# Performance work log

Hardware: AMD Instinct MI355X
Metric: run time of the kernel (lower is better)

## Reference

```python
import jax, jax.numpy as jnp
import numpy as np

K = 10

def _lrelu(v):
    return jax.nn.leaky_relu(v, negative_slope=0.2)

def _knn_idx(x, k):
    # x: [B, C, N]; returns indices of k nearest neighbors [B, N, k]
    xx = jnp.sum(x * x, axis=1, keepdims=True)          # [B,1,N]
    inner = -2.0 * jnp.einsum('bcn,bcm->bnm', x, x)     # [B,N,N]
    pd = -xx - inner - jnp.swapaxes(xx, 1, 2)           # -squared distance [B,N,N]
    _, idx = jax.lax.top_k(pd, k)
    return idx

def _graph_feature(x, k):
    # x: [B, C, N] -> edge features [B, 2C, N, k]
    idx = _knn_idx(x, k)                                # [B,N,k]
    xt = jnp.swapaxes(x, 1, 2)                          # [B,N,C]
    feat = jax.vmap(lambda xb, ib: xb[ib])(xt, idx)     # [B,N,k,C] gather
    center = xt[:, :, None, :]                          # [B,N,1,C]
    f = jnp.concatenate([feat - center,
                         jnp.broadcast_to(center, feat.shape)], axis=-1)  # [B,N,k,2C]
    return jnp.transpose(f, (0, 3, 1, 2))               # [B,2C,N,k]

def _edge_block(x, W, k):
    # conv2d 1x1 (no bias) + LeakyReLU + max over neighbors
    g = _graph_feature(x, k)                            # [B,2C,N,k]
    h = _lrelu(jnp.einsum('oc,bcnk->bonk', W, g))
    return jnp.max(h, axis=-1)                          # [B,O,N]

def setup_inputs() -> dict:
    key = jax.random.key(0)
    ks = jax.random.split(key, 9)
    def w(k_, *shape):
        fan_in = shape[-1]
        return jax.random.normal(k_, shape, dtype=jnp.float32) / np.sqrt(fan_in)
    return {
        'x':  jax.random.normal(ks[0], (8, 3, 2048), dtype=jnp.float32),
        'W1': w(ks[1], 64, 6),
        'W2': w(ks[2], 64, 128),
        'W3': w(ks[3], 128, 128),
        'W4': w(ks[4], 256, 256),
        'W5': w(ks[5], 512, 512),
        'L1': w(ks[6], 512, 1024),
        'L2': w(ks[7], 256, 512),
        'b2': jnp.zeros((256,), dtype=jnp.float32),
    }

def reference(x, W1, W2, W3, W4, W5, L1, L2, b2):
    x1 = _edge_block(x,  W1, K)   # [B,64,N]
    x2 = _edge_block(x1, W2, K)   # [B,64,N]
    x3 = _edge_block(x2, W3, K)   # [B,128,N]
    x4 = _edge_block(x3, W4, K)   # [B,256,N]
    h = jnp.concatenate([x1, x2, x3, x4], axis=1)        # [B,512,N]
    h = _lrelu(jnp.einsum('oc,bcn->bon', W5, h))         # [B,512,N]
    hmax = jnp.max(h, axis=-1)                           # [B,512]
    havg = jnp.mean(h, axis=-1)                          # [B,512]
    f = jnp.concatenate([hmax, havg], axis=1)            # [B,1024]
    f = _lrelu(f @ L1.T)                                 # [B,512]
    out = _lrelu(f @ L2.T + b2)                          # [B,256]
    return out
```

## Files before the change

### kernel.cpp

```cpp
#include <hip/hip_runtime.h>
#include <cstdint>
#include <cstddef>

constexpr int B_ = 8;
constexpr int N_ = 2048;
constexpr int K_ = 10;

typedef __attribute__((ext_vector_type(8))) short bf16x8;
typedef __attribute__((ext_vector_type(4))) float f32x4;

__device__ __forceinline__ float lrelu(float v) { return fmaxf(v, 0.2f * v); }

__device__ __forceinline__ short f2bf(float f) {
    uint32_t u = __builtin_bit_cast(uint32_t, f);
    u += 0x7fff + ((u >> 16) & 1);
    return (short)(u >> 16);
}
__device__ __forceinline__ float bf2f(short s) {
    uint32_t x = ((uint32_t)(unsigned short)s) << 16;
    return __builtin_bit_cast(float, x);
}

__global__ void k_transpose(const float* __restrict__ x, float* __restrict__ xt) {
    int i = blockIdx.x * 256 + threadIdx.x;
    if (i >= B_ * N_) return;
    int b = i / N_, n = i % N_;
#pragma unroll
    for (int c = 0; c < 3; ++c)
        xt[(size_t)i * 3 + c] = x[((size_t)b * 3 + c) * N_ + n];
}

__global__ void k_cvt(const float* __restrict__ W4, const float* __restrict__ W5,
                      short* __restrict__ Wb4, short* __restrict__ W5b) {
    int i = blockIdx.x * 256 + threadIdx.x;
    if (i < 256 * 128) {
        Wb4[i] = f2bf(W4[(size_t)(i >> 7) * 256 + (i & 127)]);
    } else {
        int k = i - 256 * 128;
        if (k < 512 * 512) W5b[k] = f2bf(W5[k]);
    }
}

__global__ void k_norms(const float* __restrict__ xt, int LD, int OFF, int C,
                        float* __restrict__ nrm) {
    int gid = blockIdx.x * 256 + threadIdx.x;
    int wid = gid >> 6;
    int lane = threadIdx.x & 63;
    if (wid >= B_ * N_) return;
    const float* row = xt + (size_t)wid * LD + OFF;
    float s = 0.f;
    for (int c = lane; c < C; c += 64) { float v = row[c]; s += v * v; }
#pragma unroll
    for (int off = 32; off; off >>= 1) s += __shfl_down(s, off);
    if (lane == 0) nrm[wid] = s;
}

__global__ __launch_bounds__(256) void k_knn3(const float* __restrict__ x,
                                              int* __restrict__ idxout) {
    __shared__ float xs[3][N_];
    __shared__ float ns[N_];
    const int b = blockIdx.x;
    const int w = threadIdx.x >> 6, lane = threadIdx.x & 63;
    const int n = blockIdx.y * 4 + w;
    for (int e = threadIdx.x; e < 3 * N_; e += 256)
        xs[e / N_][e % N_] = x[(size_t)b * 3 * N_ + e];
    __syncthreads();
    for (int m = threadIdx.x; m < N_; m += 256) {
        float a0 = xs[0][m], a1 = xs[1][m], a2 = xs[2][m];
        ns[m] = a0 * a0 + a1 * a1 + a2 * a2;
    }
    __syncthreads();
    const float q0 = xs[0][n], q1 = xs[1][n], q2 = xs[2][n];

    float sv[32];
#pragma unroll
    for (int g = 0; g < 32; ++g) {
        int m = g * 64 + lane;
        sv[g] = 2.f * (q0 * xs[0][m] + q1 * xs[1][m] + q2 * xs[2][m]) - ns[m];
    }
    float lm = sv[0];
#pragma unroll
    for (int g = 1; g < 32; ++g) lm = fmaxf(lm, sv[g]);
    float cur = lm, T = lm;
#pragma unroll
    for (int i = 0; i < K_; ++i) {
        float wm = cur;
#pragma unroll
        for (int off = 1; off < 64; off <<= 1) wm = fmaxf(wm, __shfl_xor(wm, off));
        T = wm;
        unsigned long long m = __ballot(cur == wm);
        int first = __ffsll(m) - 1;
        if (lane == first) cur = -INFINITY;
    }
    float kv[K_]; int ki[K_];
#pragma unroll
    for (int i = 0; i < K_; ++i) { kv[i] = -INFINITY; ki[i] = 0x7fffffff; }
#pragma unroll
    for (int g = 0; g < 32; ++g) {
        unsigned long long mk = __ballot(sv[g] >= T && sv[g] > kv[0]);
        while (mk) {
            int l = __ffsll(mk) - 1;
            mk &= mk - 1;
            float v = __shfl(sv[g], l);
            if (v > kv[0]) {
                kv[0] = v; ki[0] = g * 64 + l;
#pragma unroll
                for (int u = 0; u < K_ - 1; ++u)
                    if (kv[u] > kv[u + 1]) {
                        float tv = kv[u]; kv[u] = kv[u + 1]; kv[u + 1] = tv;
                        int tix = ki[u]; ki[u] = ki[u + 1]; ki[u + 1] = tix;
                    }
            }
        }
    }
    if (lane == 0) {
        int* op = idxout + ((size_t)b * N_ + n) * K_;
#pragma unroll
        for (int k = 0; k < K_; ++k) op[k] = ki[K_ - 1 - k];
    }
}

template <int C>
__global__ __launch_bounds__(256) void k_scores_mfma(const float* __restrict__ xt, int LD, int OFF,
                                                     const float* __restrict__ nrm,
                                                     float* __restrict__ S, int b0) {
    constexpr int RPC = C / 64;
    constexpr int NCH = 3 * RPC;
    constexpr int T = N_ / 64;
    __shared__ short AN[64 * 64];
    __shared__ short AM[64 * 64];
    const int bl = blockIdx.x;
    const int b = b0 + bl;
    int p = blockIdx.y;
    int r0 = 0, off = 0;
    while (off + (T - r0) <= p) { off += T - r0; ++r0; }
    const int ti = r0, tj = r0 + (p - off);
    const int n0 = ti * 64, m0 = tj * 64;
    const int t = threadIdx.x;
    const int lane = t & 63, w = t >> 6;
    const int colg = lane & 15, kg = lane >> 4;
    const float* xb = xt + ((size_t)b * N_) * LD + OFF;
    const float* nb = nrm + (size_t)b * N_;
    float* Sb = S + (size_t)bl * N_ * N_;

    f32x4 acc[4];
#pragma unroll
    for (int j = 0; j < 4; ++j) acc[j] = (f32x4){0.f, 0.f, 0.f, 0.f};

    for (int ch = 0; ch < NCH; ++ch) {
        const int region = ch / RPC;
        const int cc0 = (ch % RPC) * 64;
        __syncthreads();
#pragma unroll
        for (int e = 0; e < 4; ++e) {
            int idx = t + e * 256;
            int r = idx >> 4, q = idx & 15;
            float4 vn = *(const float4*)&xb[(size_t)(n0 + r) * LD + cc0 + q * 4];
            float4 vm = *(const float4*)&xb[(size_t)(m0 + r) * LD + cc0 + q * 4];
            float an4[4] = {vn.x, vn.y, vn.z, vn.w};
            float am4[4] = {vm.x, vm.y, vm.z, vm.w};
            short sa[4], sb[4];
#pragma unroll
            for (int c2 = 0; c2 < 4; ++c2) {
                short hn = f2bf(an4[c2]);
                short hm = f2bf(am4[c2]);
                sa[c2] = (region == 1) ? f2bf(an4[c2] - bf2f(hn)) : hn;
                sb[c2] = (region == 2) ? f2bf(am4[c2] - bf2f(hm)) : hm;
            }
            int base16 = r * 128 + (q >> 1) * 16;
            int byte = (base16 ^ ((r & 7) << 4)) + (q & 1) * 8;
            *(short4*)((char*)AN + byte) = make_short4(sa[0], sa[1], sa[2], sa[3]);
            *(short4*)((char*)AM + byte) = make_short4(sb[0], sb[1], sb[2], sb[3]);
        }
        __syncthreads();
        const int arow = w * 16 + colg;
#pragma unroll
        for (int s = 0; s < 2; ++s) {
            int abyte = (arow * 128 + s * 64 + kg * 16) ^ ((arow & 7) << 4);
            bf16x8 af = *(const bf16x8*)((const char*)AN + abyte);
#pragma unroll
            for (int j = 0; j < 4; ++j) {
                int brow = j * 16 + colg;
                int bbyte = (brow * 128 + s * 64 + kg * 16) ^ ((brow & 7) << 4);
                bf16x8 bfr = *(const bf16x8*)((const char*)AM + bbyte);
                acc[j] = __builtin_amdgcn_mfma_f32_16x16x32_bf16(af, bfr, acc[j], 0, 0, 0);
            }
        }
    }
#pragma unroll
    for (int j = 0; j < 4; ++j) {
        float nm = nb[m0 + j * 16 + colg];
#pragma unroll
        for (int r = 0; r < 4; ++r) {
            int row = n0 + w * 16 + kg * 4 + r;
            Sb[(size_t)row * N_ + m0 + j * 16 + colg] = 2.f * acc[j][r] - nm;
        }
    }
    if (ti != tj) {
#pragma unroll
        for (int r = 0; r < 4; ++r) {
            int nrow = n0 + w * 16 + kg * 4 + r;
            float nn = nb[nrow];
#pragma unroll
            for (int j = 0; j < 4; ++j)
                Sb[(size_t)(m0 + j * 16 + colg) * N_ + nrow] = 2.f * acc[j][r] - nn;
        }
    }
}

__global__ __launch_bounds__(256) void k_topk(const float* __restrict__ S,
                                              int* __restrict__ idxout, int b0) {
    const int bl = blockIdx.x, b = b0 + bl;
    const int wv = threadIdx.x >> 6, lane = threadIdx.x & 63;
    const int n = blockIdx.y * 4 + wv;
    const float* row = S + (size_t)bl * N_ * N_ + (size_t)n * N_;

    float sv[32];
#pragma unroll
    for (int g = 0; g < 32; ++g) sv[g] = __builtin_nontemporal_load(&row[g * 64 + lane]);

    float lm = sv[0];
#pragma unroll
    for (int g = 1; g < 32; ++g) lm = fmaxf(lm, sv[g]);

    float cur = lm, T = lm;
#pragma unroll
    for (int i = 0; i < K_; ++i) {
        float wm = cur;
#pragma unroll
        for (int off = 1; off < 64; off <<= 1) wm = fmaxf(wm, __shfl_xor(wm, off));
        T = wm;
        unsigned long long m = __ballot(cur == wm);
        int first = __ffsll(m) - 1;
        if (lane == first) cur = -INFINITY;
    }

    float kv[K_]; int ki[K_];
#pragma unroll
    for (int i = 0; i < K_; ++i) { kv[i] = -INFINITY; ki[i] = 0x7fffffff; }

#pragma unroll
    for (int g = 0; g < 32; ++g) {
        unsigned long long mk = __ballot(sv[g] >= T && sv[g] > kv[0]);
        while (mk) {
            int l = __ffsll(mk) - 1;
            mk &= mk - 1;
            float v = __shfl(sv[g], l);
            if (v > kv[0]) {
                kv[0] = v; ki[0] = g * 64 + l;
#pragma unroll
                for (int u = 0; u < K_ - 1; ++u)
                    if (kv[u] > kv[u + 1]) {
                        float tv = kv[u]; kv[u] = kv[u + 1]; kv[u + 1] = tv;
                        int tix = ki[u]; ki[u] = ki[u + 1]; ki[u + 1] = tix;
                    }
            }
        }
    }
    if (lane == 0) {
        int* op = idxout + ((size_t)b * N_ + n) * K_;
#pragma unroll
        for (int k = 0; k < K_; ++k) op[k] = ki[K_ - 1 - k];
    }
}

template <int C, int O>
__global__ __launch_bounds__(256) void k_center(const float* __restrict__ xt, int LD, int OFF,
                                                const float* __restrict__ W,
                                                float* __restrict__ tbuf) {
    constexpr int KC = (C == 3) ? 4 : 32;
    __shared__ __align__(16) float XT[64][36];
    __shared__ __align__(16) float WDT[KC][68];
    const int b = blockIdx.x;
    const int n0 = blockIdx.y * 64;
    const int ob = blockIdx.z * 64;
    const int t = threadIdx.x;
    const int tn = t & 15, to = t >> 4;
    const float* xb = xt + ((size_t)b * N_) * LD + OFF;
    float4 acc[4];
#pragma unroll
    for (int i = 0; i < 4; ++i) acc[i] = make_float4(0, 0, 0, 0);
    for (int c0 = 0; c0 < C; c0 += KC) {
        __syncthreads();
        for (int e = t; e < 64 * KC; e += 256) {
            int r = e / KC, cc = e % KC;
            XT[r][cc] = (C == 3) ? ((cc < 3) ? xb[(size_t)(n0 + r) * LD + cc] : 0.f)
                                 : xb[(size_t)(n0 + r) * LD + c0 + cc];
        }
        for (int e = t; e < 64 * KC; e += 256) {
            int oo = e / KC, cc = e % KC;
            float wd, wc;
            if (C == 3) {
                wd = (cc < 3) ? W[(ob + oo) * 6 + cc] : 0.f;
                wc = (cc < 3) ? W[(ob + oo) * 6 + 3 + cc] : 0.f;
            } else {
                wd = W[(size_t)(ob + oo) * (2 * C) + c0 + cc];
                wc = W[(size_t)(ob + oo) * (2 * C) + C + c0 + cc];
            }
            WDT[cc][oo] = wc - wd;
        }
        __syncthreads();
#pragma unroll 4
        for (int cc = 0; cc < KC; ++cc) {
            float4 w4 = *(const float4*)&WDT[cc][to * 4];
#pragma unroll
            for (int i = 0; i < 4; ++i) {
                float a = XT[tn * 4 + i][cc];
                acc[i].x += a * w4.x; acc[i].y += a * w4.y;
                acc[i].z += a * w4.z; acc[i].w += a * w4.w;
            }
        }
    }
#pragma unroll
    for (int i = 0; i < 4; ++i)
        *(float4*)&tbuf[((size_t)b * N_ + n0 + tn * 4 + i) * O + ob + to * 4] = acc[i];
}

template <int C, int O>
__global__ __launch_bounds__(256) void k_conv(const float* __restrict__ xt, int LDI, int OFFI,
                                              const int* __restrict__ idx,
                                              const float* __restrict__ W,
                                              const float* __restrict__ tbuf,
                                              float* __restrict__ hout, int OFFO) {
    constexpr int KC = (C == 3) ? 4 : 32;
    __shared__ __align__(16) float A[160][36];
    __shared__ __align__(16) float WT[KC][68];
    __shared__ int nb_s[160];
    const int b = blockIdx.x;
    const int n0 = blockIdx.y * 16;
    const int t = threadIdx.x;
    const int p = t >> 4, og = t & 15;
    if (t < 160) nb_s[t] = idx[((size_t)b * N_ + n0 + t / K_) * K_ + (t % K_)];
    const float* xb = xt + ((size_t)b * N_) * LDI + OFFI;

    for (int ob = 0; ob < O; ob += 64) {
        float4 acc[K_];
#pragma unroll
        for (int j = 0; j < K_; ++j) acc[j] = make_float4(0, 0, 0, 0);
        for (int c0 = 0; c0 < C; c0 += KC) {
            __syncthreads();
            if (C == 3) {
                for (int e = t; e < 160 * 4; e += 256) {
                    int r = e / 4, cc = e % 4;
                    A[r][cc] = (cc < 3) ? xb[(size_t)nb_s[r] * LDI + cc] : 0.f;
                }
            } else {
                for (int e = t; e < 160 * 8; e += 256) {
                    int r = e / 8, c4 = e % 8;
                    *(float4*)&A[r][c4 * 4] =
                        *(const float4*)&xb[(size_t)nb_s[r] * LDI + c0 + c4 * 4];
                }
            }
            for (int e = t; e < 64 * KC; e += 256) {
                int oo = e / KC, cc = e % KC;
                float w;
                if (C == 3) w = (cc < 3) ? W[(ob + oo) * 6 + cc] : 0.f;
                else        w = W[(size_t)(ob + oo) * (2 * C) + c0 + cc];
                WT[cc][oo] = w;
            }
            __syncthreads();
#pragma unroll 4
            for (int cc = 0; cc < KC; ++cc) {
                float4 w4 = *(const float4*)&WT[cc][og * 4];
#pragma unroll
                for (int j = 0; j < K_; ++j) {
                    float a = A[p * K_ + j][cc];
                    acc[j].x += a * w4.x; acc[j].y += a * w4.y;
                    acc[j].z += a * w4.z; acc[j].w += a * w4.w;
                }
            }
        }
        float4 tv = *(const float4*)&tbuf[((size_t)b * N_ + n0 + p) * O + ob + og * 4];
        float4 mx = acc[0];
#pragma unroll
        for (int j = 1; j < K_; ++j) {
            mx.x = fmaxf(mx.x, acc[j].x); mx.y = fmaxf(mx.y, acc[j].y);
            mx.z = fmaxf(mx.z, acc[j].z); mx.w = fmaxf(mx.w, acc[j].w);
        }
        float4 r;
        r.x = lrelu(mx.x + tv.x); r.y = lrelu(mx.y + tv.y);
        r.z = lrelu(mx.z + tv.z); r.w = lrelu(mx.w + tv.w);
        *(float4*)&hout[((size_t)b * N_ + n0 + p) * 512 + OFFO + ob + og * 4] = r;
    }
}

__global__ __launch_bounds__(256) void k_conv4_mfma(const float* __restrict__ hcat,
                                                    const int* __restrict__ idx,
                                                    const short* __restrict__ Wb,
                                                    const float* __restrict__ tbuf,
                                                    float* __restrict__ hout) {
    __shared__ short Ab[160 * 128];
    __shared__ int nb_s[160];
    const int b = blockIdx.x;
    const int n0 = blockIdx.y * 16;
    const int t = threadIdx.x;
    const int lane = t & 63, wv = t >> 6;
    const int colg = lane & 15, kg = lane >> 4;
    if (t < 160) nb_s[t] = idx[((size_t)b * N_ + n0 + t / K_) * K_ + (t % K_)];
    __syncthreads();
    for (int e = t; e < 160 * 32; e += 256) {
        int r = e >> 5, q = e & 31;
        const float4 v = *(const float4*)&hcat[((size_t)b * N_ + nb_s[r]) * 512 + 128 + q * 4];
        short4 s4 = { f2bf(v.x), f2bf(v.y), f2bf(v.z), f2bf(v.w) };
        int byte = r * 256 + ((q * 8) ^ (((r / K_) & 7) << 4));
        *(short4*)((char*)Ab + byte) = s4;
    }
    bf16x8 bf[4][4];
    const int ob = wv * 64;
#pragma unroll
    for (int nt = 0; nt < 4; ++nt)
#pragma unroll
        for (int ks = 0; ks < 4; ++ks)
            bf[nt][ks] = *(const bf16x8*)&Wb[(size_t)(ob + nt * 16 + colg) * 128 + ks * 32 + kg * 8];
    __syncthreads();

    f32x4 macc[4];
#pragma unroll
    for (int nt = 0; nt < 4; ++nt)
        macc[nt] = (f32x4){-INFINITY, -INFINITY, -INFINITY, -INFINITY};

    const int arow = colg * K_;
    const int aswz = (colg & 7) << 4;
#pragma unroll
    for (int j = 0; j < K_; ++j) {
        f32x4 acc[4];
#pragma unroll
        for (int nt = 0; nt < 4; ++nt) acc[nt] = (f32x4){0.f, 0.f, 0.f, 0.f};
#pragma unroll
        for (int ks = 0; ks < 4; ++ks) {
            int byte = (arow + j) * 256 + (((ks * 32 + kg * 8) * 2) ^ aswz);
            bf16x8 af = *(const bf16x8*)((const char*)Ab + byte);
#pragma unroll
            for (int nt = 0; nt < 4; ++nt)
                acc[nt] = __builtin_amdgcn_mfma_f32_16x16x32_bf16(af, bf[nt][ks], acc[nt], 0, 0, 0);
        }
#pragma unroll
        for (int nt = 0; nt < 4; ++nt) {
            macc[nt].x = fmaxf(macc[nt].x, acc[nt].x);
            macc[nt].y = fmaxf(macc[nt].y, acc[nt].y);
            macc[nt].z = fmaxf(macc[nt].z, acc[nt].z);
            macc[nt].w = fmaxf(macc[nt].w, acc[nt].w);
        }
    }
#pragma unroll
    for (int nt = 0; nt < 4; ++nt)
#pragma unroll
        for (int r = 0; r < 4; ++r) {
            int p = kg * 4 + r;
            int o = ob + nt * 16 + colg;
            float v = macc[nt][r] + tbuf[((size_t)b * N_ + n0 + p) * 256 + o];
            hout[((size_t)b * N_ + n0 + p) * 512 + 256 + o] = lrelu(v);
        }
}

__global__ __launch_bounds__(256) void k_final_mfma(const float* __restrict__ hcat,
                                                    const short* __restrict__ W5b,
                                                    float* __restrict__ pmax,
                                                    float* __restrict__ psum) {
    __shared__ short Ab[64 * 128];
    const int b = blockIdx.x, nc = blockIdx.y, obk = blockIdx.z;
    const int n0 = nc * 64, ob = obk * 64;
    const int t = threadIdx.x, lane = t & 63, wv = t >> 6;
    const int colg = lane & 15, kg = lane >> 4;
    const int o = ob + wv * 16 + colg;

    f32x4 acc[4];
#pragma unroll
    for (int mt = 0; mt < 4; ++mt) acc[mt] = (f32x4){0.f, 0.f, 0.f, 0.f};

    for (int kc = 0; kc < 4; ++kc) {
        __syncthreads();
        for (int e = t; e < 64 * 32; e += 256) {
            int r = e >> 5, q = e & 31;
            const float4 v = *(const float4*)&hcat[((size_t)b * N_ + n0 + r) * 512 + kc * 128 + q * 4];
            short4 s4 = { f2bf(v.x), f2bf(v.y), f2bf(v.z), f2bf(v.w) };
            int byte = r * 256 + ((q * 8) ^ ((r & 7) << 4));
            *(short4*)((char*)Ab + byte) = s4;
        }
        __syncthreads();
#pragma unroll
        for (int ks = 0; ks < 4; ++ks) {
            bf16x8 bfrag = *(const bf16x8*)&W5b[(size_t)o * 512 + kc * 128 + ks * 32 + kg * 8];
#pragma unroll
            for (int mt = 0; mt < 4; ++mt) {
                int row = mt * 16 + colg;
                int byte = row * 256 + (((ks * 32 + kg * 8) * 2) ^ ((row & 7) << 4));
                bf16x8 af = *(const bf16x8*)((const char*)Ab + byte);
                acc[mt] = __builtin_amdgcn_mfma_f32_16x16x32_bf16(af, bfrag, acc[mt], 0, 0, 0);
            }
        }
    }
    float mx = -INFINITY, sm = 0.f;
#pragma unroll
    for (int mt = 0; mt < 4; ++mt)
#pragma unroll
        for (int r = 0; r < 4; ++r) {
            float v = lrelu(acc[mt][r]);
            mx = fmaxf(mx, v); sm += v;
        }
    mx = fmaxf(mx, __shfl_xor(mx, 16)); sm += __shfl_xor(sm, 16);
    mx = fmaxf(mx, __shfl_xor(mx, 32)); sm += __shfl_xor(sm, 32);
    if (lane < 16) {
        pmax[((size_t)b * 512 + ob + wv * 16 + lane) * 32 + nc] = mx;
        psum[((size_t)b * 512 + ob + wv * 16 + lane) * 32 + nc] = sm;
    }
}

__global__ __launch_bounds__(256) void k_pool(const float* __restrict__ pmax,
                                              const float* __restrict__ psum,
                                              float* __restrict__ f) {
    int i = blockIdx.x * 256 + threadIdx.x;
    if (i >= B_ * 512) return;
    int b = i >> 9, o = i & 511;
    const float* pm = pmax + (size_t)i * 32;
    const float* ps = psum + (size_t)i * 32;
    float mm = -INFINITY, ss = 0.f;
#pragma unroll
    for (int q = 0; q < 32; ++q) { mm = fmaxf(mm, pm[q]); ss += ps[q]; }
    f[(size_t)b * 1024 + o] = mm;
    f[(size_t)b * 1024 + 512 + o] = ss * (1.0f / 2048.0f);
}

__global__ __launch_bounds__(256) void k_fc1(const float* __restrict__ f,
                                             const float* __restrict__ L1,
                                             float* __restrict__ f1) {
    __shared__ float fs[8][1024];
    const int t = threadIdx.x, lane = t & 63, w = t >> 6;
    for (int e = t; e < 2048; e += 256)
        *(float4*)&fs[0][e * 4] = *(const float4*)&f[e * 4];
    __syncthreads();
    const int o = blockIdx.x * 4 + w;
    float acc[8];
#pragma unroll
    for (int b = 0; b < 8; ++b) acc[b] = 0.f;
    const float* Lrow = L1 + (size_t)o * 1024;
#pragma unroll
    for (int e = 0; e < 16; ++e) {
        float wv = Lrow[e * 64 + lane];
#pragma unroll
        for (int b = 0; b < 8; ++b) acc[b] += wv * fs[b][e * 64 + lane];
    }
#pragma unroll
    for (int off = 32; off; off >>= 1)
#pragma unroll
        for (int b = 0; b < 8; ++b) acc[b] += __shfl_xor(acc[b], off);
#pragma unroll
    for (int b = 0; b < 8; ++b)
        if (lane == b) f1[(size_t)b * 512 + o] = lrelu(acc[b]);
}

__global__ __launch_bounds__(256) void k_fc2(const float* __restrict__ f1,
                                             const float* __restrict__ L2,
                                             const float* __restrict__ b2,
                                             float* __restrict__ out) {
    __shared__ float fs[8][512];
    const int t = threadIdx.x, lane = t & 63, w = t >> 6;
    for (int e = t; e < 1024; e += 256)
        *(float4*)&fs[0][e * 4] = *(const float4*)&f1[e * 4];
    __syncthreads();
    const int o = blockIdx.x * 4 + w;
    float acc[8];
#pragma unroll
    for (int b = 0; b < 8; ++b) acc[b] = 0.f;
    const float* Lrow = L2 + (size_t)o * 512;
#pragma unroll
    for (int e = 0; e < 8; ++e) {
        float wv = Lrow[e * 64 + lane];
#pragma unroll
        for (int b = 0; b < 8; ++b) acc[b] += wv * fs[b][e * 64 + lane];
    }
#pragma unroll
    for (int off = 32; off; off >>= 1)
#pragma unroll
        for (int b = 0; b < 8; ++b) acc[b] += __shfl_xor(acc[b], off);
    float bb = b2[o];
#pragma unroll
    for (int b = 0; b < 8; ++b)
        if (lane == b) out[(size_t)b * 256 + o] = lrelu(acc[b] + bb);
}

extern "C" void kernel_launch(void* const* d_in, const int* in_sizes, int n_in,
                              void* d_out, int out_size, void* d_ws, size_t ws_size,
                              hipStream_t stream) {
    (void)in_sizes; (void)n_in; (void)out_size;
    const float* x  = (const float*)d_in[0];
    const float* W1 = (const float*)d_in[1];
    const float* W2 = (const float*)d_in[2];
    const float* W3 = (const float*)d_in[3];
    const float* W4 = (const float*)d_in[4];
    const float* W5 = (const float*)d_in[5];
    const float* L1 = (const float*)d_in[6];
    const float* L2 = (const float*)d_in[7];
    const float* b2 = (const float*)d_in[8];
    float* out = (float*)d_out;

    float* ws   = (float*)d_ws;
    float* xt   = ws;
    float* nrm  = xt + (size_t)B_ * N_ * 3;
    int*   idxb = (int*)(nrm + (size_t)B_ * N_);
    float* tb   = (float*)(idxb + (size_t)B_ * N_ * K_);
    float* hcat = tb + (size_t)B_ * N_ * 256;
    float* pmax = hcat + (size_t)B_ * N_ * 512;
    float* psum = pmax + (size_t)B_ * 512 * 32;
    short* wb4  = (short*)(psum + (size_t)B_ * 512 * 32);
    short* w5b  = wb4 + 256 * 128;
    float* fbuf = (float*)(w5b + 512 * 512);
    float* f1b  = fbuf + 8192;
    float* scor = f1b + 4096;

    const size_t base_f = 49152 + 16384 + 163840 + 4194304 + 8388608 +
                          131072 + 131072 + 16384 + 131072 + 8192 + 4096;
    const size_t nsq = (size_t)N_ * N_;
    size_t avail = (ws_size / 4 > base_f) ? (ws_size / 4 - base_f) : 0;
    int CH = 1;
    if (avail >= 8 * nsq) CH = 8;
    else if (avail >= 4 * nsq) CH = 4;
    else if (avail >= 2 * nsq) CH = 2;

    constexpr int TP = (N_ / 64) * (N_ / 64 + 1) / 2;

    dim3 blk(256);
    k_transpose<<<dim3((B_ * N_ + 255) / 256), blk, 0, stream>>>(x, xt);
    k_cvt<<<dim3((256 * 128 + 512 * 512 + 255) / 256), blk, 0, stream>>>(W4, W5, wb4, w5b);

    k_knn3<<<dim3(B_, N_ / 4), blk, 0, stream>>>(x, idxb);
    k_center<3, 64><<<dim3(B_, N_ / 64, 1), blk, 0, stream>>>(xt, 3, 0, W1, tb);
    k_conv<3, 64><<<dim3(B_, N_ / 16), blk, 0, stream>>>(xt, 3, 0, idxb, W1, tb, hcat, 0);

    k_norms<<<dim3(B_ * N_ / 4), blk, 0, stream>>>(hcat, 512, 0, 64, nrm);
    for (int b0 = 0; b0 < B_; b0 += CH) {
        k_scores_mfma<64><<<dim3(CH, TP), blk, 0, stream>>>(hcat, 512, 0, nrm, scor, b0);
        k_topk<<<dim3(CH, N_ / 4), blk, 0, stream>>>(scor, idxb, b0);
    }
    k_center<64, 64><<<dim3(B_, N_ / 64, 1), blk, 0, stream>>>(hcat, 512, 0, W2, tb);
    k_conv<64, 64><<<dim3(B_, N_ / 16), blk, 0, stream>>>(hcat, 512, 0, idxb, W2, tb, hcat, 64);

    k_norms<<<dim3(B_ * N_ / 4), blk, 0, stream>>>(hcat, 512, 64, 64, nrm);
    for (int b0 = 0; b0 < B_; b0 += CH) {
        k_scores_mfma<64><<<dim3(CH, TP), blk, 0, stream>>>(hcat, 512, 64, nrm, scor, b0);
        k_topk<<<dim3(CH, N_ / 4), blk, 0, stream>>>(scor, idxb, b0);
    }
    k_center<64, 128><<<dim3(B_, N_ / 64, 2), blk, 0, stream>>>(hcat, 512, 64, W3, tb);
    k_conv<64, 128><<<dim3(B_, N_ / 16), blk, 0, stream>>>(hcat, 512, 64, idxb, W3, tb, hcat, 128);

    k_norms<<<dim3(B_ * N_ / 4), blk, 0, stream>>>(hcat, 512, 128, 128, nrm);
    for (int b0 = 0; b0 < B_; b0 += CH) {
        k_scores_mfma<128><<<dim3(CH, TP), blk, 0, stream>>>(hcat, 512, 128, nrm, scor, b0);
        k_topk<<<dim3(CH, N_ / 4), blk, 0, stream>>>(scor, idxb, b0);
    }
    k_center<128, 256><<<dim3(B_, N_ / 64, 4), blk, 0, stream>>>(hcat, 512, 128, W4, tb);
    k_conv4_mfma<<<dim3(B_, N_ / 16), blk, 0, stream>>>(hcat, idxb, wb4, tb, hcat);

    k_final_mfma<<<dim3(B_, 32, 8), blk, 0, stream>>>(hcat, w5b, pmax, psum);
    k_pool<<<dim3(B_ * 512 / 256), blk, 0, stream>>>(pmax, psum, fbuf);
    k_fc1<<<dim3(128), blk, 0, stream>>>(fbuf, L1, f1b);
    k_fc2<<<dim3(64), blk, 0, stream>>>(f1b, L2, b2, out);
}
```

Before: 544.9 us.

## Fuse kNN score GEMM with streaming top-k, split columns and merge

Replaces the separate score kernel, which wrote the full N×N distance matrix, and the top-k kernel that read it back, with one kernel. Each block computes 64-row score tiles with MFMA and keeps a running per-row top-10 in shared memory. Columns are split across CS=2 blocks and a small merge kernel combines the partial lists. This removes the large score-matrix traffic and the batching loop, but it drops the symmetric tile reuse, so the dot-product work doubles, and it adds a serial per-row insertion loop within each wave.

```diff
diff --git a/kernel.cpp b/kernel.cpp
--- a/kernel.cpp
+++ b/kernel.cpp
@@ -120,147 +120,139 @@
     }
 }
 
-template <int C>
-__global__ __launch_bounds__(256) void k_scores_mfma(const float* __restrict__ xt, int LD, int OFF,
-                                                     const float* __restrict__ nrm,
-                                                     float* __restrict__ S, int b0) {
+template <int C, int CS>
+__global__ __launch_bounds__(256) void k_knn_fmfma(const float* __restrict__ xt, int LD, int OFF,
+                                                   const float* __restrict__ nrm,
+                                                   float* __restrict__ pv, int* __restrict__ pi) {
     constexpr int RPC = C / 64;
     constexpr int NCH = 3 * RPC;
-    constexpr int T = N_ / 64;
+    constexpr int COLS = N_ / CS;
+    constexpr int NT = COLS / 64;
     __shared__ short AN[64 * 64];
     __shared__ short AM[64 * 64];
-    const int bl = blockIdx.x;
-    const int b = b0 + bl;
-    int p = blockIdx.y;
-    int r0 = 0, off = 0;
-    while (off + (T - r0) <= p) { off += T - r0; ++r0; }
-    const int ti = r0, tj = r0 + (p - off);
-    const int n0 = ti * 64, m0 = tj * 64;
+    __shared__ float SCN[4][16][65];
+    __shared__ float KV[64][10];
+    __shared__ int   KI[64][10];
+    const int b = blockIdx.x;
+    const int n0 = blockIdx.y * 64;
+    const int cs = blockIdx.z;
     const int t = threadIdx.x;
     const int lane = t & 63, w = t >> 6;
     const int colg = lane & 15, kg = lane >> 4;
     const float* xb = xt + ((size_t)b * N_) * LD + OFF;
     const float* nb = nrm + (size_t)b * N_;
-    float* Sb = S + (size_t)bl * N_ * N_;
-
-    f32x4 acc[4];
-#pragma unroll
-    for (int j = 0; j < 4; ++j) acc[j] = (f32x4){0.f, 0.f, 0.f, 0.f};
-
-    for (int ch = 0; ch < NCH; ++ch) {
-        const int region = ch / RPC;
-        const int cc0 = (ch % RPC) * 64;
-        __syncthreads();
-#pragma unroll
-        for (int e = 0; e < 4; ++e) {
-            int idx = t + e * 256;
-            int r = idx >> 4, q = idx & 15;
-            float4 vn = *(const float4*)&xb[(size_t)(n0 + r) * LD + cc0 + q * 4];
-            float4 vm = *(const float4*)&xb[(size_t)(m0 + r) * LD + cc0 + q * 4];
-            float an4[4] = {vn.x, vn.y, vn.z, vn.w};
-            float am4[4] = {vm.x, vm.y, vm.z, vm.w};
-            short sa[4], sb[4];
-#pragma unroll
-            for (int c2 = 0; c2 < 4; ++c2) {
-                short hn = f2bf(an4[c2]);
-                short hm = f2bf(am4[c2]);
-                sa[c2] = (region == 1) ? f2bf(an4[c2] - bf2f(hn)) : hn;
-                sb[c2] = (region == 2) ? f2bf(am4[c2] - bf2f(hm)) : hm;
-            }
-            int base16 = r * 128 + (q >> 1) * 16;
-            int byte = (base16 ^ ((r & 7) << 4)) + (q & 1) * 8;
-            *(short4*)((char*)AN + byte) = make_short4(sa[0], sa[1], sa[2], sa[3]);
-            *(short4*)((char*)AM + byte) = make_short4(sb[0], sb[1], sb[2], sb[3]);
-        }
-        __syncthreads();
-        const int arow = w * 16 + colg;
-#pragma unroll
-        for (int s = 0; s < 2; ++s) {
-            int abyte = (arow * 128 + s * 64 + kg * 16) ^ ((arow & 7) << 4);
-            bf16x8 af = *(const bf16x8*)((const char*)AN + abyte);
-#pragma unroll
-            for (int j = 0; j < 4; ++j) {
-                int brow = j * 16 + colg;
-                int bbyte = (brow * 128 + s * 64 + kg * 16) ^ ((brow & 7) << 4);
-                bf16x8 bfr = *(const bf16x8*)((const char*)AM + bbyte);
-                acc[j] = __builtin_amdgcn_mfma_f32_16x16x32_bf16(af, bfr, acc[j], 0, 0, 0);
-            }
-        }
-    }
-#pragma unroll
-    for (int j = 0; j < 4; ++j) {
-        float nm = nb[m0 + j * 16 + colg];
-#pragma unroll
-        for (int r = 0; r < 4; ++r) {
-            int row = n0 + w * 16 + kg * 4 + r;
-            Sb[(size_t)row * N_ + m0 + j * 16 + colg] = 2.f * acc[j][r] - nm;
-        }
-    }
-    if (ti != tj) {
-#pragma unroll
-        for (int r = 0; r < 4; ++r) {
-            int nrow = n0 + w * 16 + kg * 4 + r;
-            float nn = nb[nrow];
-#pragma unroll
-            for (int j = 0; j < 4; ++j)
-                Sb[(size_t)(m0 + j * 16 + colg) * N_ + nrow] = 2.f * acc[j][r] - nn;
-        }
-    }
-}
-
-__global__ __launch_bounds__(256) void k_topk(const float* __restrict__ S,
-                                              int* __restrict__ idxout, int b0) {
-    const int bl = blockIdx.x, b = b0 + bl;
-    const int wv = threadIdx.x >> 6, lane = threadIdx.x & 63;
-    const int n = blockIdx.y * 4 + wv;
-    const float* row = S + (size_t)bl * N_ * N_ + (size_t)n * N_;
-
-    float sv[32];
-#pragma unroll
-    for (int g = 0; g < 32; ++g) sv[g] = __builtin_nontemporal_load(&row[g * 64 + lane]);
-
-    float lm = sv[0];
-#pragma unroll
-    for (int g = 1; g < 32; ++g) lm = fmaxf(lm, sv[g]);
-
-    float cur = lm, T = lm;
-#pragma unroll
-    for (int i = 0; i < K_; ++i) {
-        float wm = cur;
-#pragma unroll
-        for (int off = 1; off < 64; off <<= 1) wm = fmaxf(wm, __shfl_xor(wm, off));
-        T = wm;
-        unsigned long long m = __ballot(cur == wm);
-        int first = __ffsll(m) - 1;
-        if (lane == first) cur = -INFINITY;
-    }
-
-    float kv[K_]; int ki[K_];
-#pragma unroll
-    for (int i = 0; i < K_; ++i) { kv[i] = -INFINITY; ki[i] = 0x7fffffff; }
-
-#pragma unroll
-    for (int g = 0; g < 32; ++g) {
-        unsigned long long mk = __ballot(sv[g] >= T && sv[g] > kv[0]);
-        while (mk) {
-            int l = __ffsll(mk) - 1;
-            mk &= mk - 1;
-            float v = __shfl(sv[g], l);
-            if (v > kv[0]) {
-                kv[0] = v; ki[0] = g * 64 + l;
-#pragma unroll
-                for (int u = 0; u < K_ - 1; ++u)
-                    if (kv[u] > kv[u + 1]) {
-                        float tv = kv[u]; kv[u] = kv[u + 1]; kv[u + 1] = tv;
-                        int tix = ki[u]; ki[u] = ki[u + 1]; ki[u + 1] = tix;
+
+    for (int e = t; e < 640; e += 256) { KV[e / 10][e % 10] = -INFINITY; KI[e / 10][e % 10] = 0x7fffffff; }
+
+    for (int tile = 0; tile < NT; ++tile) {
+        const int mt0 = cs * COLS + tile * 64;
+        f32x4 acc[4];
+#pragma unroll
+        for (int j = 0; j < 4; ++j) acc[j] = (f32x4){0.f, 0.f, 0.f, 0.f};
+
+        for (int ch = 0; ch < NCH; ++ch) {
+            const int region = ch / RPC;
+            const int cc0 = (ch % RPC) * 64;
+            __syncthreads();
+#pragma unroll
+            for (int e = 0; e < 4; ++e) {
+                int idx = t + e * 256;
+                int r = idx >> 4, q = idx & 15;
+                float4 vn = *(const float4*)&xb[(size_t)(n0 + r) * LD + cc0 + q * 4];
+                float4 vm = *(const float4*)&xb[(size_t)(mt0 + r) * LD + cc0 + q * 4];
+                float an4[4] = {vn.x, vn.y, vn.z, vn.w};
+                float am4[4] = {vm.x, vm.y, vm.z, vm.w};
+                short sa[4], sb[4];
+#pragma unroll
+                for (int c2 = 0; c2 < 4; ++c2) {
+                    short hn = f2bf(an4[c2]);
+                    short hm = f2bf(am4[c2]);
+                    sa[c2] = (region == 1) ? f2bf(an4[c2] - bf2f(hn)) : hn;
+                    sb[c2] = (region == 2) ? f2bf(am4[c2] - bf2f(hm)) : hm;
+                }
+                int base16 = r * 128 + (q >> 1) * 16;
+                int byte = (base16 ^ ((r & 7) << 4)) + (q & 1) * 8;
+                *(short4*)((char*)AN + byte) = make_short4(sa[0], sa[1], sa[2], sa[3]);
+                *(short4*)((char*)AM + byte) = make_short4(sb[0], sb[1], sb[2], sb[3]);
+            }
+            __syncthreads();
+            const int arow = w * 16 + colg;
+#pragma unroll
+            for (int s = 0; s < 2; ++s) {
+                int abyte = (arow * 128 + s * 64 + kg * 16) ^ ((arow & 7) << 4);
+                bf16x8 af = *(const bf16x8*)((const char*)AN + abyte);
+#pragma unroll
+                for (int j = 0; j < 4; ++j) {
+                    int brow = j * 16 + colg;
+                    int bbyte = (brow * 128 + s * 64 + kg * 16) ^ ((brow & 7) << 4);
+                    bf16x8 bfr = *(const bf16x8*)((const char*)AM + bbyte);
+                    acc[j] = __builtin_amdgcn_mfma_f32_16x16x32_bf16(af, bfr, acc[j], 0, 0, 0);
+                }
+            }
+        }
+#pragma unroll
+        for (int j = 0; j < 4; ++j) {
+            float nm = nb[mt0 + j * 16 + colg];
+#pragma unroll
+            for (int r = 0; r < 4; ++r)
+                SCN[w][kg * 4 + r][j * 16 + colg] = 2.f * acc[j][r] - nm;
+        }
+        for (int row = 0; row < 16; ++row) {
+            const int gr = w * 16 + row;
+            float v = SCN[w][row][lane];
+            float kv0 = KV[gr][0];
+            unsigned long long mk = __ballot(v > kv0);
+            while (mk) {
+                int l = __ffsll(mk) - 1;
+                mk &= mk - 1;
+                float vv = __shfl(v, l);
+                kv0 = KV[gr][0];
+                if (vv > kv0) {
+                    float slot = (lane < 10) ? KV[gr][lane] : 0.f;
+                    unsigned long long lessm = __ballot(lane < 10 && slot < vv);
+                    int p = (int)__popcll(lessm);
+                    if (lane < 10) {
+                        float nv; int ni;
+                        if (lane < p - 1)      { nv = KV[gr][lane + 1]; ni = KI[gr][lane + 1]; }
+                        else if (lane == p - 1){ nv = vv; ni = mt0 + l; }
+                        else                   { nv = slot; ni = KI[gr][lane]; }
+                        KV[gr][lane] = nv; KI[gr][lane] = ni;
                     }
-            }
-        }
-    }
-    if (lane == 0) {
-        int* op = idxout + ((size_t)b * N_ + n) * K_;
-#pragma unroll
-        for (int k = 0; k < K_; ++k) op[k] = ki[K_ - 1 - k];
+                }
+            }
+        }
+    }
+    __syncthreads();
+    if (t < 64) {
+        float* opv = pv + (((size_t)b * N_ + n0 + t) * CS + cs) * K_;
+        int*   opi = pi + (((size_t)b * N_ + n0 + t) * CS + cs) * K_;
+#pragma unroll
+        for (int k = 0; k < K_; ++k) { opv[k] = KV[t][9 - k]; opi[k] = KI[t][9 - k]; }
+    }
+}
+
+template <int CS>
+__global__ __launch_bounds__(256) void k_kmerge(const float* __restrict__ pv,
+                                                const int* __restrict__ pi,
+                                                int* __restrict__ idxout) {
+    int row = blockIdx.x * 256 + threadIdx.x;
+    if (row >= B_ * N_) return;
+    const float* rv = pv + (size_t)row * CS * K_;
+    const int*   ri = pi + (size_t)row * CS * K_;
+    int p[CS];
+#pragma unroll
+    for (int q = 0; q < CS; ++q) p[q] = 0;
+    int* op = idxout + (size_t)row * K_;
+    for (int k = 0; k < K_; ++k) {
+        float bv = -INFINITY; int bi = 0x7fffffff, bq = 0;
+#pragma unroll
+        for (int q = 0; q < CS; ++q) {
+            float v = rv[q * K_ + p[q]];
+            int id = ri[q * K_ + p[q]];
+            if (v > bv || (v == bv && id < bi)) { bv = v; bi = id; bq = q; }
+        }
+        op[k] = bi;
+        ++p[bq];
     }
 }
 
@@ -582,7 +574,7 @@
 extern "C" void kernel_launch(void* const* d_in, const int* in_sizes, int n_in,
                               void* d_out, int out_size, void* d_ws, size_t ws_size,
                               hipStream_t stream) {
-    (void)in_sizes; (void)n_in; (void)out_size;
+    (void)in_sizes; (void)n_in; (void)out_size; (void)ws_size;
     const float* x  = (const float*)d_in[0];
     const float* W1 = (const float*)d_in[1];
     const float* W2 = (const float*)d_in[2];
@@ -593,6 +585,8 @@
     const float* L2 = (const float*)d_in[7];
     const float* b2 = (const float*)d_in[8];
     float* out = (float*)d_out;
+
+    constexpr int CS = 2;
 
     float* ws   = (float*)d_ws;
     float* xt   = ws;
@@ -606,18 +600,8 @@
     short* w5b  = wb4 + 256 * 128;
     float* fbuf = (float*)(w5b + 512 * 512);
     float* f1b  = fbuf + 8192;
-    float* scor = f1b + 4096;
-
-    const size_t base_f = 49152 + 16384 + 163840 + 4194304 + 8388608 +
-                          131072 + 131072 + 16384 + 131072 + 8192 + 4096;
-    const size_t nsq = (size_t)N_ * N_;
-    size_t avail = (ws_size / 4 > base_f) ? (ws_size / 4 - base_f) : 0;
-    int CH = 1;
-    if (avail >= 8 * nsq) CH = 8;
-    else if (avail >= 4 * nsq) CH = 4;
-    else if (avail >= 2 * nsq) CH = 2;
-
-    constexpr int TP = (N_ / 64) * (N_ / 64 + 1) / 2;
+    float* pv   = f1b + 4096;
+    int*   pi   = (int*)(pv + (size_t)B_ * N_ * CS * K_);
 
     dim3 blk(256);
     k_transpose<<<dim3((B_ * N_ + 255) / 256), blk, 0, stream>>>(x, xt);
@@ -628,26 +612,20 @@
     k_conv<3, 64><<<dim3(B_, N_ / 16), blk, 0, stream>>>(xt, 3, 0, idxb, W1, tb, hcat, 0);
 
     k_norms<<<dim3(B_ * N_ / 4), blk, 0, stream>>>(hcat, 512, 0, 64, nrm);
-    for (int b0 = 0; b0 < B_; b0 += CH) {
-        k_scores_mfma<64><<<dim3(CH, TP), blk, 0, stream>>>(hcat, 512, 0, nrm, scor, b0);
-        k_topk<<<dim3(CH, N_ / 4), blk, 0, stream>>>(scor, idxb, b0);
-    }
+    k_knn_fmfma<64, CS><<<dim3(B_, N_ / 64, CS), blk, 0, stream>>>(hcat, 512, 0, nrm, pv, pi);
+    k_kmerge<CS><<<dim3(B_ * N_ / 256), blk, 0, stream>>>(pv, pi, idxb);
     k_center<64, 64><<<dim3(B_, N_ / 64, 1), blk, 0, stream>>>(hcat, 512, 0, W2, tb);
     k_conv<64, 64><<<dim3(B_, N_ / 16), blk, 0, stream>>>(hcat, 512, 0, idxb, W2, tb, hcat, 64);
 
     k_norms<<<dim3(B_ * N_ / 4), blk, 0, stream>>>(hcat, 512, 64, 64, nrm);
-    for (int b0 = 0; b0 < B_; b0 += CH) {
-        k_scores_mfma<64><<<dim3(CH, TP), blk, 0, stream>>>(hcat, 512, 64, nrm, scor, b0);
-        k_topk<<<dim3(CH, N_ / 4), blk, 0, stream>>>(scor, idxb, b0);
-    }
+    k_knn_fmfma<64, CS><<<dim3(B_, N_ / 64, CS), blk, 0, stream>>>(hcat, 512, 64, nrm, pv, pi);
+    k_kmerge<CS><<<dim3(B_ * N_ / 256), blk, 0, stream>>>(pv, pi, idxb);
     k_center<64, 128><<<dim3(B_, N_ / 64, 2), blk, 0, stream>>>(hcat, 512, 64, W3, tb);
     k_conv<64, 128><<<dim3(B_, N_ / 16), blk, 0, stream>>>(hcat, 512, 64, idxb, W3, tb, hcat, 128);
 
     k_norms<<<dim3(B_ * N_ / 4), blk, 0, stream>>>(hcat, 512, 128, 128, nrm);
-    for (int b0 = 0; b0 < B_; b0 += CH) {
-        k_scores_mfma<128><<<dim3(CH, TP), blk, 0, stream>>>(hcat, 512, 128, nrm, scor, b0);
-        k_topk<<<dim3(CH, N_ / 4), blk, 0, stream>>>(scor, idxb, b0);
-    }
+    k_knn_fmfma<128, CS><<<dim3(B_, N_ / 64, CS), blk, 0, stream>>>(hcat, 512, 128, nrm, pv, pi);
+    k_kmerge<CS><<<dim3(B_ * N_ / 256), blk, 0, stream>>>(pv, pi, idxb);
     k_center<128, 256><<<dim3(B_, N_ / 64, 4), blk, 0, stream>>>(hcat, 512, 128, W4, tb);
     k_conv4_mfma<<<dim3(B_, N_ / 16), blk, 0, stream>>>(hcat, idxb, wb4, tb, hcat);
 
```

Result: slower. 1.368 ms (+151.0%).

## Run edge conv layers 2 and 3 on MFMA with split-bf16 precision

Applied to the files above, without the earlier changes.

Replaces the scalar FP32 neighbor convolution for blocks 2 and 3 with an MFMA kernel. Gathered neighbor features and weights are each split into bf16 high and low parts, and three bf16 MFMA products (hi*hi, lo*hi, hi*lo) approximate FP32 accuracy. The max over neighbors and the center-term add are fused into the epilogue. This adds a small weight pre-conversion kernel and swizzled LDS staging, and uses three times the MFMA work in exchange for matrix-core throughput in place of VALU FMAs.

```diff
diff --git a/kernel.cpp b/kernel.cpp
--- a/kernel.cpp
+++ b/kernel.cpp
@@ -38,6 +38,22 @@
     } else {
         int k = i - 256 * 128;
         if (k < 512 * 512) W5b[k] = f2bf(W5[k]);
+    }
+}
+
+__global__ void k_cvt2(const float* __restrict__ W2, const float* __restrict__ W3,
+                       short* __restrict__ w2h, short* __restrict__ w2l,
+                       short* __restrict__ w3h, short* __restrict__ w3l) {
+    int i = blockIdx.x * 256 + threadIdx.x;
+    if (i < 64 * 64) {
+        float v = W2[(size_t)(i >> 6) * 128 + (i & 63)];
+        short h = f2bf(v);
+        w2h[i] = h; w2l[i] = f2bf(v - bf2f(h));
+    } else if (i < 64 * 64 + 128 * 64) {
+        int k = i - 64 * 64;
+        float v = W3[(size_t)(k >> 6) * 128 + (k & 63)];
+        short h = f2bf(v);
+        w3h[k] = h; w3l[k] = f2bf(v - bf2f(h));
     }
 }
 
@@ -384,6 +400,103 @@
     }
 }
 
+template <int O>
+__global__ __launch_bounds__(256) void k_conv23_mfma(const float* __restrict__ hcat, int OFFI,
+                                                     const int* __restrict__ idx,
+                                                     const short* __restrict__ Wh,
+                                                     const short* __restrict__ Wl,
+                                                     const float* __restrict__ tbuf,
+                                                     float* __restrict__ hout, int OFFO) {
+    constexpr int CT = O / 64;
+    __shared__ short Ah[160 * 64];
+    __shared__ short Al[160 * 64];
+    __shared__ int nb_s[160];
+    const int b = blockIdx.x;
+    const int n0 = blockIdx.y * 16;
+    const int t = threadIdx.x;
+    const int lane = t & 63, wv = t >> 6;
+    const int colg = lane & 15, kg = lane >> 4;
+    if (t < 160) nb_s[t] = idx[((size_t)b * N_ + n0 + t / K_) * K_ + (t % K_)];
+    __syncthreads();
+    for (int e = t; e < 160 * 16; e += 256) {
+        int r = e >> 4, q = e & 15;
+        const float4 v = *(const float4*)&hcat[((size_t)b * N_ + nb_s[r]) * 512 + OFFI + q * 4];
+        float a4[4] = {v.x, v.y, v.z, v.w};
+        short sh[4], sl[4];
+#pragma unroll
+        for (int c2 = 0; c2 < 4; ++c2) {
+            sh[c2] = f2bf(a4[c2]);
+            sl[c2] = f2bf(a4[c2] - bf2f(sh[c2]));
+        }
+        int byte = r * 128 + ((q * 8) ^ (((r / K_) & 7) << 4));
+        *(short4*)((char*)Ah + byte) = make_short4(sh[0], sh[1], sh[2], sh[3]);
+        *(short4*)((char*)Al + byte) = make_short4(sl[0], sl[1], sl[2], sl[3]);
+    }
+    bf16x8 bh[CT][2], blo[CT][2];
+    const int obase = wv * (O / 4);
+#pragma unroll
+    for (int ct = 0; ct < CT; ++ct)
+#pragma unroll
+        for (int ks = 0; ks < 2; ++ks) {
+            int o = obase + ct * 16 + colg;
+            bh[ct][ks]  = *(const bf16x8*)&Wh[(size_t)o * 64 + ks * 32 + kg * 8];
+            blo[ct][ks] = *(const bf16x8*)&Wl[(size_t)o * 64 + ks * 32 + kg * 8];
+        }
+    __syncthreads();
+
+    f32x4 macc[CT];
+#pragma unroll
+    for (int ct = 0; ct < CT; ++ct)
+        macc[ct] = (f32x4){-INFINITY, -INFINITY, -INFINITY, -INFINITY};
+
+    const int aswz = (colg & 7) << 4;
+#pragma unroll
+    for (int j = 0; j < K_; ++j) {
+        const int arow = colg * K_ + j;
+        bf16x8 afh[2], afl[2];
+#pragma unroll
+        for (int ks = 0; ks < 2; ++ks) {
+            int byte = arow * 128 + ((ks * 64 + kg * 16) ^ aswz);
+            afh[ks] = *(const bf16x8*)((const char*)Ah + byte);
+            afl[ks] = *(const bf16x8*)((const char*)Al + byte);
+        }
+        f32x4 acc[CT];
+#pragma unroll
+        for (int ct = 0; ct < CT; ++ct) acc[ct] = (f32x4){0.f, 0.f, 0.f, 0.f};
+#pragma unroll
+        for (int ks = 0; ks < 2; ++ks)
+#pragma unroll
+            for (int ct = 0; ct < CT; ++ct)
+                acc[ct] = __builtin_amdgcn_mfma_f32_16x16x32_bf16(afh[ks], bh[ct][ks], acc[ct], 0, 0, 0);
+#pragma unroll
+        for (int ks = 0; ks < 2; ++ks)
+#pragma unroll
+            for (int ct = 0; ct < CT; ++ct)
+                acc[ct] = __builtin_amdgcn_mfma_f32_16x16x32_bf16(afl[ks], bh[ct][ks], acc[ct], 0, 0, 0);
+#pragma unroll
+        for (int ks = 0; ks < 2; ++ks)
+#pragma unroll
+            for (int ct = 0; ct < CT; ++ct)
+                acc[ct] = __builtin_amdgcn_mfma_f32_16x16x32_bf16(afh[ks], blo[ct][ks], acc[ct], 0, 0, 0);
+#pragma unroll
+        for (int ct = 0; ct < CT; ++ct) {
+            macc[ct].x = fmaxf(macc[ct].x, acc[ct].x);
+            macc[ct].y = fmaxf(macc[ct].y, acc[ct].y);
+            macc[ct].z = fmaxf(macc[ct].z, acc[ct].z);
+            macc[ct].w = fmaxf(macc[ct].w, acc[ct].w);
+        }
+    }
+#pragma unroll
+    for (int ct = 0; ct < CT; ++ct)
+#pragma unroll
+        for (int r = 0; r < 4; ++r) {
+            int p = kg * 4 + r;
+            int o = obase + ct * 16 + colg;
+            float v = macc[ct][r] + tbuf[((size_t)b * N_ + n0 + p) * O + o];
+            hout[((size_t)b * N_ + n0 + p) * 512 + OFFO + o] = lrelu(v);
+        }
+}
+
 __global__ __launch_bounds__(256) void k_conv4_mfma(const float* __restrict__ hcat,
                                                     const int* __restrict__ idx,
                                                     const short* __restrict__ Wb,
@@ -604,12 +717,16 @@
     float* psum = pmax + (size_t)B_ * 512 * 32;
     short* wb4  = (short*)(psum + (size_t)B_ * 512 * 32);
     short* w5b  = wb4 + 256 * 128;
-    float* fbuf = (float*)(w5b + 512 * 512);
+    short* w2h  = w5b + 512 * 512;
+    short* w2l  = w2h + 64 * 64;
+    short* w3h  = w2l + 64 * 64;
+    short* w3l  = w3h + 128 * 64;
+    float* fbuf = (float*)(w3l + 128 * 64);
     float* f1b  = fbuf + 8192;
     float* scor = f1b + 4096;
 
     const size_t base_f = 49152 + 16384 + 163840 + 4194304 + 8388608 +
-                          131072 + 131072 + 16384 + 131072 + 8192 + 4096;
+                          131072 + 131072 + 16384 + 131072 + 12288 + 8192 + 4096;
     const size_t nsq = (size_t)N_ * N_;
     size_t avail = (ws_size / 4 > base_f) ? (ws_size / 4 - base_f) : 0;
     int CH = 1;
@@ -622,6 +739,7 @@
     dim3 blk(256);
     k_transpose<<<dim3((B_ * N_ + 255) / 256), blk, 0, stream>>>(x, xt);
     k_cvt<<<dim3((256 * 128 + 512 * 512 + 255) / 256), blk, 0, stream>>>(W4, W5, wb4, w5b);
+    k_cvt2<<<dim3((64 * 64 + 128 * 64 + 255) / 256), blk, 0, stream>>>(W2, W3, w2h, w2l, w3h, w3l);
 
     k_knn3<<<dim3(B_, N_ / 4), blk, 0, stream>>>(x, idxb);
     k_center<3, 64><<<dim3(B_, N_ / 64, 1), blk, 0, stream>>>(xt, 3, 0, W1, tb);
@@ -633,7 +751,7 @@
         k_topk<<<dim3(CH, N_ / 4), blk, 0, stream>>>(scor, idxb, b0);
     }
     k_center<64, 64><<<dim3(B_, N_ / 64, 1), blk, 0, stream>>>(hcat, 512, 0, W2, tb);
-    k_conv<64, 64><<<dim3(B_, N_ / 16), blk, 0, stream>>>(hcat, 512, 0, idxb, W2, tb, hcat, 64);
+    k_conv23_mfma<64><<<dim3(B_, N_ / 16), blk, 0, stream>>>(hcat, 0, idxb, w2h, w2l, tb, hcat, 64);
 
     k_norms<<<dim3(B_ * N_ / 4), blk, 0, stream>>>(hcat, 512, 64, 64, nrm);
     for (int b0 = 0; b0 < B_; b0 += CH) {
@@ -641,7 +759,7 @@
         k_topk<<<dim3(CH, N_ / 4), blk, 0, stream>>>(scor, idxb, b0);
     }
     k_center<64, 128><<<dim3(B_, N_ / 64, 2), blk, 0, stream>>>(hcat, 512, 64, W3, tb);
-    k_conv<64, 128><<<dim3(B_, N_ / 16), blk, 0, stream>>>(hcat, 512, 64, idxb, W3, tb, hcat, 128);
+    k_conv23_mfma<128><<<dim3(B_, N_ / 16), blk, 0, stream>>>(hcat, 64, idxb, w3h, w3l, tb, hcat, 128);
 
     k_norms<<<dim3(B_ * N_ / 4), blk, 0, stream>>>(hcat, 512, 128, 128, nrm);
     for (int b0 = 0; b0 < B_; b0 += CH) {
```

New measurement: 524.0 us. 3.8% less time.
